# Kernel tuning notes

Measured on AMD Instinct MI355X. Metric: run time of the kernel, lower is better.

Reference implementation:

```python
import jax, jax.numpy as jnp
import numpy as np

N_HEAD = 8
TOKEN_CODIM = 4   # mixer token codimension; attention uses per-channel tokens (codim 1)
TEMP = 1.0
EPS = 1e-5


def instance_norm(x, w=None, b=None):
    # InstanceNorm2d: normalize each (sample, channel) over spatial dims
    mu = jnp.mean(x, axis=(-2, -1), keepdims=True)
    var = jnp.var(x, axis=(-2, -1), keepdims=True)
    y = (x - mu) * jax.lax.rsqrt(var + EPS)
    if w is not None:
        y = y * w[:, None, None] + b[:, None, None]
    return y


def spectral_conv(x, wr, wi, bias, out_hw):
    # x: (B, Cin, H, W); weight (Cin, Cout, m1, m2) complex; fft_norm='forward'
    B, Cin, H, W = x.shape
    Ho, Wo = out_hw
    w = wr + 1j * wi
    m1, m2 = wr.shape[2], wr.shape[3]
    h = m1 // 2
    xf = jnp.fft.rfft2(x, norm='forward')                  # (B, Cin, H, W//2+1)
    top = jnp.einsum('bixy,ioxy->boxy', xf[:, :, :h, :m2], w[:, :, :h])
    bot = jnp.einsum('bixy,ioxy->boxy', xf[:, :, H - h:, :m2], w[:, :, h:])
    of = jnp.zeros((B, wr.shape[1], Ho, Wo // 2 + 1), dtype=xf.dtype)
    of = of.at[:, :, :h, :m2].set(top)
    of = of.at[:, :, Ho - h:, :m2].set(bot)
    return jnp.fft.irfft2(of, s=(Ho, Wo), norm='forward') + bias[:, None, None]


def fft_resample(x, Ho, Wo):
    # Fourier-truncation resampling (used for the skip branch when the conv rescales)
    B, C, H, W = x.shape
    xf = jnp.fft.rfft2(x, norm='forward')
    h, wc = Ho // 2, Wo // 2 + 1
    of = jnp.zeros((B, C, Ho, wc), dtype=xf.dtype)
    of = of.at[:, :, :h].set(xf[:, :, :h, :wc])
    of = of.at[:, :, Ho - h:].set(xf[:, :, H - h:, :wc])
    return jnp.fft.irfft2(of, s=(Ho, Wo), norm='forward')


def fno_layer(x, wr, wi, bias, sw, sb, out_hw, norm=False, act=False):
    # one FNOBlocks layer: spectral conv (+optional instance norm) + 1x1 linear skip (+act)
    skip = jnp.einsum('bihw,oi->bohw', x, sw) + sb[:, None, None]
    if out_hw != tuple(x.shape[-2:]):
        skip = fft_resample(skip, *out_hw)
    xf = spectral_conv(x, wr, wi, bias, out_hw)
    if norm:
        xf = instance_norm(xf)
    y = xf + skip
    return jax.nn.gelu(y, approximate=False) if act else y


def to_heads(z, b):
    # '(b t) (a d) h w -> b a t (d h w)'
    bt, ad, h, w = z.shape
    t = bt // b
    z = z.reshape(b, t, N_HEAD, ad // N_HEAD, h, w)
    return jnp.transpose(z, (0, 2, 1, 3, 4, 5)).reshape(b, N_HEAD, t, -1)


def setup_inputs():
    key = jax.random.key(0)
    ks = jax.random.split(key, 12)
    b, C, H, W = 2, 128, 128, 128
    f = jax.random.normal
    return dict(
        x=f(ks[0], (b, C, H, W), jnp.float32),
        norm1_w=jnp.ones((1,)), norm1_b=jnp.zeros((1,)),
        kqv_wr=f(ks[1], (3, 1, N_HEAD, 16, 8)) * 0.02,
        kqv_wi=f(ks[2], (3, 1, N_HEAD, 16, 8)) * 0.02,
        kqv_bias=f(ks[3], (3, N_HEAD)) * 0.02,
        kqv_sw=f(ks[4], (3, N_HEAD, 1)) * 0.5,
        kqv_sb=jnp.zeros((3, N_HEAD)),
        p_wr=f(ks[5], (N_HEAD, 1, 32, 16)) * 0.02,
        p_wi=f(ks[6], (N_HEAD, 1, 32, 16)) * 0.02,
        p_bias=jnp.zeros((1,)),
        p_sw=f(ks[7], (1, N_HEAD)) * (1.0 / np.sqrt(N_HEAD)),
        p_sb=jnp.zeros((1,)),
        attn_norm_w=jnp.ones((1,)), attn_norm_b=jnp.zeros((1,)),
        norm2_w=jnp.ones((TOKEN_CODIM,)), norm2_b=jnp.zeros((TOKEN_CODIM,)),
        mix_wr=f(ks[8], (2, TOKEN_CODIM, TOKEN_CODIM, 32, 16)) * 0.02,
        mix_wi=f(ks[9], (2, TOKEN_CODIM, TOKEN_CODIM, 32, 16)) * 0.02,
        mix_bias=jnp.zeros((2, TOKEN_CODIM)),
        mix_sw=f(ks[10], (2, TOKEN_CODIM, TOKEN_CODIM)) * 0.5,
        mix_sb=jnp.zeros((2, TOKEN_CODIM)),
        mon_w=jnp.ones((TOKEN_CODIM,)), mon_b=jnp.zeros((TOKEN_CODIM,)),
    )


def reference(x, norm1_w, norm1_b, kqv_wr, kqv_wi, kqv_bias, kqv_sw, kqv_sb,
              p_wr, p_wi, p_bias, p_sw, p_sb, attn_norm_w, attn_norm_b,
              norm2_w, norm2_b, mix_wr, mix_wi, mix_bias, mix_sw, mix_sb,
              mon_w, mon_b):
    b, C, H, W = x.shape
    tokens = x.reshape(b * C, 1, H, W)                     # per-channel tokens
    tok_n = instance_norm(tokens, norm1_w, norm1_b)        # norm1

    # K, Q downsampled by scale=2; V at full resolution (kqv_modes = n_modes // 2)
    k = fno_layer(tok_n, kqv_wr[0], kqv_wi[0], kqv_bias[0], kqv_sw[0], kqv_sb[0], (H // 2, W // 2))
    q = fno_layer(tok_n, kqv_wr[1], kqv_wi[1], kqv_bias[1], kqv_sw[1], kqv_sb[1], (H // 2, W // 2))
    v = fno_layer(tok_n, kqv_wr[2], kqv_wi[2], kqv_bias[2], kqv_sw[2], kqv_sb[2], (H, W))

    kh, qh, vh = to_heads(k, b), to_heads(q, b), to_heads(v, b)
    scores = jnp.einsum('bati,basi->bats', qh, kh) / (np.float32(np.sqrt(kh.shape[-1])) * TEMP)
    probs = jax.nn.softmax(scores, axis=-1)                # (b, heads, t, t)
    attn = jnp.einsum('bats,basi->bati', probs, vh)        # (b, heads, C, H*W)
    attn = attn.reshape(b, N_HEAD, C, 1, H, W).transpose(0, 2, 1, 3, 4, 5).reshape(b * C, N_HEAD, H, W)

    attn = fno_layer(attn, p_wr, p_wi, p_bias, p_sw, p_sb, (H, W))   # proj heads -> codim 1
    attn = instance_norm(attn + tokens, attn_norm_w, attn_norm_b)

    # regroup channels into mixer tokens of codimension 4
    attn = attn.reshape(b * (C // TOKEN_CODIM), TOKEN_CODIM, H, W)
    h0 = instance_norm(attn, norm2_w, norm2_b)
    h1 = fno_layer(h0, mix_wr[0], mix_wi[0], mix_bias[0], mix_sw[0], mix_sb[0], (H, W), norm=True, act=True)
    h2 = fno_layer(h1, mix_wr[1], mix_wi[1], mix_bias[1], mix_sw[1], mix_sb[1], (H, W), norm=True)
    out = instance_norm(h2, mon_w, mon_b) + attn
    return out.reshape(b, C, H, W)
```

## Files before the change

kernel.cpp:

```cpp
#include <hip/hip_runtime.h>
#include <math.h>


#define NT 2112

__device__ __forceinline__ void blockReduce2(float& a, float& b, float* red){
  const int tid = threadIdx.x, n = blockDim.x;
  red[tid] = a; red[n+tid] = b;
  __syncthreads();
  for(int off=n>>1; off>0; off>>=1){
    if(tid<off){ red[tid]+=red[tid+off]; red[n+tid]+=red[n+tid+off]; }
    __syncthreads();
  }
  a = red[0]; b = red[n];
  __syncthreads();
}

__device__ __forceinline__ float2 cmul_add(float2 acc, float2 w, float2 x){
  acc.x += w.x*x.x - w.y*x.y;
  acc.y += w.x*x.y + w.y*x.x;
  return acc;
}

__global__ void k_tables(float2* __restrict__ CS){
  int a = blockIdx.x, b = threadIdx.x;
  int p = (a*b)&127;
  float t = (float)p * (1.0f/64.0f);
  CS[a*128+b] = make_float2(cospif(t), sinpif(t));
}

__global__ __launch_bounds__(256) void k_instats(
    const float* __restrict__ xin, const float* __restrict__ n1w,
    const float* __restrict__ n1b, float* __restrict__ a1, float* __restrict__ b1)
{
  __shared__ float red[512];
  const int m = blockIdx.x, t = threadIdx.x;
  const float* xp = xin + (size_t)m*16384;
  float s1=0.f, s2=0.f;
  for(int i=t;i<4096;i+=256){
    float4 v = ((const float4*)xp)[i];
    s1 += v.x+v.y+v.z+v.w;
    s2 += v.x*v.x+v.y*v.y+v.z*v.z+v.w*v.w;
  }
  blockReduce2(s1,s2,red);
  if(t==0){
    float mu = s1*(1.0f/16384.0f);
    float var = s2*(1.0f/16384.0f)-mu*mu;
    float a = n1w[0]*rsqrtf(var+1e-5f);
    a1[m] = a; b1[m] = n1b[0] - mu*a;
  }
}

__global__ __launch_bounds__(256) void k_p1(
    const float* __restrict__ xin, float* __restrict__ R1r, float* __restrict__ R1i,
    const float2* __restrict__ CS)
{
  __shared__ float xl[32*129];
  __shared__ float2 csl[4224];
  const int bid = blockIdx.x;
  const int m = bid>>2, yt = bid&3;
  const int t = threadIdx.x;
  for(int i=t;i<4224;i+=256) csl[i] = CS[i];
  {
    const float4* xp4 = (const float4*)(xin + (size_t)m*16384 + yt*4096);
    for(int i4=t;i4<1024;i4+=256){
      float4 v = xp4[i4];
      int y = i4>>5, n = (i4&31)*4;
      xl[y*129+n]=v.x; xl[y*129+n+1]=v.y; xl[y*129+n+2]=v.z; xl[y*129+n+3]=v.w;
    }
  }
  __syncthreads();
  const int yl = t&31, cg = t>>5;
  const int nc = (cg==0)?5:4;
  float ar[5]={0,0,0,0,0}, ai[5]={0,0,0,0,0};
  for(int n=0;n<128;n++){
    float xv = xl[yl*129+n];
    #pragma unroll
    for(int k=0;k<5;k++){
      if(k<nc){
        float2 cs = csl[(cg+8*k)*128+n];
        ar[k] += xv*cs.x;
        ai[k] -= xv*cs.y;
      }
    }
  }
  __syncthreads();
  #pragma unroll
  for(int k=0;k<5;k++){
    if(k<nc){
      int c = cg+8*k;
      xl[yl*33+c] = ar[k];
      xl[1056 + yl*33+c] = ai[k];
    }
  }
  __syncthreads();
  const int gb = m*4224 + yt*1056;
  for(int idx=t; idx<2112; idx+=256){
    if(idx<1056) R1r[gb+idx] = xl[idx];
    else         R1i[gb+idx-1056] = xl[idx];
  }
}

__global__ __launch_bounds__(704) void k_p2(
    const float* __restrict__ R1r, const float* __restrict__ R1i,
    const float2* __restrict__ CS, const float* __restrict__ a1,
    const float* __restrict__ n1b,
    float2* __restrict__ Xt2, float2* __restrict__ Xp)
{
  __shared__ float2 Rl[128*34];
  const int m = blockIdx.x, t = threadIdx.x;
  for(int idx=t; idx<4224; idx+=704){
    int y = idx/33, c = idx - y*33;
    Rl[y*34+c] = make_float2(R1r[m*4224+idx], R1i[m*4224+idx]);
  }
  __syncthreads();
  const float sc = a1[m]*(1.0f/16384.0f);
  const int r = t&63;
  const int ky = (r<32)? r : r+64;
  #pragma unroll
  for(int k=0;k<3;k++){
    int c = (t>>6) + 11*k;
    float ar=0.f, ai=0.f;
    for(int y=0;y<128;y++){
      float2 Rv = Rl[y*34+c];
      float2 cs = CS[128 + ((ky*y)&127)];
      ar += Rv.x*cs.x + Rv.y*cs.y;
      ai += Rv.y*cs.x - Rv.x*cs.y;
    }
    int j = r*33 + c;
    float vr = ar*sc, vi = ai*sc;
    if(j==0){ vr = n1b[0]; vi = 0.f; }
    Xt2[m*NT+j] = make_float2(vr, vi);
    if(c<16 && (r<16 || r>=48)){
      int rp = (r<16)? r : r-32;
      Xp[m*512 + rp*16 + c] = make_float2(vr, vi);
    }
  }
}

__global__ __launch_bounds__(256) void k_build_k(
  const float2* __restrict__ Xt2,
  const float* __restrict__ kqv_wr, const float* __restrict__ kqv_wi,
  const float* __restrict__ kqv_bias, const float* __restrict__ kqv_sw,
  const float* __restrict__ kqv_sb,
  float2* __restrict__ Kc)
{
  __shared__ float2 T[2112];
  __shared__ float2 Ks[2112];
  const int bid = blockIdx.x;
  const int m = bid & 255, o = bid >> 8;
  const int tid = threadIdx.x;
  for(int j=tid;j<2112;j+=256) T[j] = Xt2[m*NT+j];
  __syncthreads();
  const float swK = kqv_sw[o];
  const float swQ = kqv_sw[8+o];
  for(int j=tid;j<2112;j+=256){
    int r = j/33, c = j - r*33;
    float2 X = T[j];
    float2 K = make_float2(swK*X.x, swK*X.y);
    if(c<8){
      int wrow = (r<8)? r : ((r>=56)? r-48 : -1);
      if(wrow>=0)
        K = cmul_add(K, make_float2(kqv_wr[(o*16+wrow)*8+c], kqv_wi[(o*16+wrow)*8+c]), X);
    }
    if(j==0) K.x += kqv_bias[o] + kqv_sb[o];
    Ks[j] = K;
  }
  __syncthreads();
  const size_t ob = ((size_t)(m*8+o))*NT;
  for(int j=tid;j<2112;j+=256){
    int r = j/33, c = j - r*33;
    float2 K = Ks[j];
    float wsc = 128.0f;
    if(c==0 || c==32){
      int pj = ((64-r)&63)*33 + c;
      float2 K2 = Ks[pj];
      K = make_float2(0.5f*(K.x+K2.x), 0.5f*(K.y-K2.y));
      wsc = 64.0f;
    }
    float ar = swQ, ai = 0.f;
    if(c<8){
      int wrow = (r<8)? r : ((r>=56)? r-48 : -1);
      if(wrow>=0){ ar += kqv_wr[((8+o)*16+wrow)*8+c]; ai += kqv_wi[((8+o)*16+wrow)*8+c]; }
    }
    float2 out = make_float2(wsc*(ar*K.x + ai*K.y), wsc*(ar*K.y - ai*K.x));
    if(j==0) out = make_float2(0.f, 0.f);
    Kc[ob+j] = out;
  }
}

__global__ __launch_bounds__(256) void k_scores(
  const float2* __restrict__ Xt2, const float2* __restrict__ Kc,
  float* __restrict__ Pp)
{
  __shared__ float Qs[64*52];
  __shared__ float Ks[64*52];
  const int bid = blockIdx.x;
  const int fq = bid&15, st = (bid>>4)&1, tt = (bid>>5)&1, h = (bid>>6)&7, b = bid>>9;
  const int t = threadIdx.x;
  const int tg = t>>4, sg = t&15;
  const int t0 = tt*64, s0 = st*64;
  const int f2base = fq*132;
  float acc[4][4];
  #pragma unroll
  for(int i=0;i<4;i++)
    #pragma unroll
    for(int j=0;j<4;j++) acc[i][j]=0.f;
  for(int sub=0; sub<6; sub++){
    __syncthreads();
    const int fo = f2base + sub*22;
    for(int idx=t; idx<1408; idx+=256){
      int rl = idx/22, f2 = idx - rl*22;
      float2 q = Xt2[(size_t)(b*128 + t0+rl)*NT + fo + f2];
      ((float2*)(Qs + rl*52))[f2] = q;
      float2 kk = Kc[((size_t)((b*128 + s0+rl)*8+h))*NT + fo + f2];
      ((float2*)(Ks + rl*52))[f2] = kk;
    }
    __syncthreads();
    #pragma unroll
    for(int f4=0; f4<11; f4++){
      float4 qv[4], kv[4];
      #pragma unroll
      for(int i=0;i<4;i++) qv[i] = *(const float4*)&Qs[(tg+16*i)*52 + f4*4];
      #pragma unroll
      for(int j=0;j<4;j++) kv[j] = *(const float4*)&Ks[(sg+16*j)*52 + f4*4];
      #pragma unroll
      for(int i=0;i<4;i++)
        #pragma unroll
        for(int j=0;j<4;j++)
          acc[i][j] += qv[i].x*kv[j].x + qv[i].y*kv[j].y
                     + qv[i].z*kv[j].z + qv[i].w*kv[j].w;
    }
  }
  #pragma unroll
  for(int i=0;i<4;i++){
    int tg2 = t0 + tg + 16*i;
    #pragma unroll
    for(int j=0;j<4;j++){
      int s = s0 + sg + 16*j;
      Pp[(size_t)fq*262144 + ((size_t)((b*8+h)*128+tg2))*128 + s] = acc[i][j];
    }
  }
}

__global__ __launch_bounds__(64) void k_softmax(const float* __restrict__ Pp,
                                                float* __restrict__ P){
  const int row = blockIdx.x, tid = threadIdx.x;
  size_t o = (size_t)row*128;
  float v0=0.f, v1=0.f;
  #pragma unroll
  for(int q=0;q<16;q++){
    v0 += Pp[(size_t)q*262144 + o + tid];
    v1 += Pp[(size_t)q*262144 + o + tid + 64];
  }
  float mx = fmaxf(v0,v1);
  for(int off=32; off; off>>=1) mx = fmaxf(mx, __shfl_xor(mx, off));
  float e0 = expf(v0-mx), e1 = expf(v1-mx);
  float s = e0+e1;
  for(int off=32; off; off>>=1) s += __shfl_xor(s, off);
  float inv = 1.0f/s;
  P[o+tid] = e0*inv; P[o+tid+64] = e1*inv;
}

__global__ __launch_bounds__(256) void k_peff(const float* __restrict__ P,
   const float* __restrict__ p_sw, const float* __restrict__ kqv_sw,
   const float* __restrict__ a1, float* __restrict__ PAT)
{
  const int i = blockIdx.x*256 + threadIdx.x;
  const int b = i>>14, rem = i&16383;
  const int tch = rem>>7, s = rem&127;
  float acc=0.f;
  for(int hh=0; hh<8; hh++){
    float a = p_sw[hh]*kqv_sw[16+hh];
    acc += a * P[(((size_t)(b*8+hh))<<14) + rem];
  }
  PAT[((size_t)(b*128+s))*128 + tch] = acc * a1[b*128+s];
}

__global__ __launch_bounds__(128) void k_pbeta(const float* __restrict__ P,
   const float* __restrict__ p_sw, const float* __restrict__ kqv_sw,
   const float* __restrict__ b1, float* __restrict__ pbeta)
{
  __shared__ float red[128];
  const int bid = blockIdx.x;
  const int b = bid>>7, tch = bid&127;
  const int s = threadIdx.x;
  float acc=0.f;
  for(int hh=0; hh<8; hh++){
    float a = p_sw[hh]*kqv_sw[16+hh];
    acc += a * P[((size_t)((b*8+hh)*128+tch))*128 + s];
  }
  acc *= b1[b*128+s];
  red[s] = acc; __syncthreads();
  for(int off=64; off>0; off>>=1){
    if(s<off) red[s]+=red[s+off];
    __syncthreads();
  }
  if(s==0) pbeta[bid] = red[0];
}

__global__ __launch_bounds__(256) void k_zp(const float* __restrict__ P,
  const float* __restrict__ Xp, float* __restrict__ Zc)
{
  __shared__ float Pt[32*17];
  __shared__ float Xs[32*256];
  const int bid = blockIdx.x;
  const int b = bid>>8;
  const int r8 = bid&255;
  const int jt = r8>>6, o = (r8>>3)&7, ct = r8&7;
  const int t = threadIdx.x;
  const int tc = t>>6, tj = t&63;
  const int c0 = ct*16;
  float4 acc[4];
  #pragma unroll
  for(int k=0;k<4;k++) acc[k] = make_float4(0.f,0.f,0.f,0.f);
  for(int scn=0; scn<4; scn++){
    __syncthreads();
    for(int idx=t; idx<512; idx+=256){
      int sl = idx&31, cl = idx>>5;
      Pt[sl*17+cl] = P[((size_t)((b*8+o)*128 + c0+cl))*128 + scn*32+sl];
    }
    for(int q=t; q<2048; q+=256){
      int sl = q>>6, p4 = q&63;
      ((float4*)Xs)[q] = ((const float4*)Xp)[((size_t)(b*128 + scn*32+sl))*256 + jt*64 + p4];
    }
    __syncthreads();
    for(int sl=0; sl<32; sl++){
      float4 xv = ((const float4*)Xs)[sl*64+tj];
      #pragma unroll
      for(int k=0;k<4;k++){
        float pa = Pt[sl*17 + tc*4+k];
        acc[k].x += pa*xv.x; acc[k].y += pa*xv.y;
        acc[k].z += pa*xv.z; acc[k].w += pa*xv.w;
      }
    }
  }
  #pragma unroll
  for(int k=0;k<4;k++){
    ((float4*)Zc)[((size_t)((b*8+o)*128 + c0+tc*4+k))*256 + jt*64 + tj] = acc[k];
  }
}

__global__ __launch_bounds__(256) void k_corr(
  const float* __restrict__ Zc,
  const float* __restrict__ kqv_wr, const float* __restrict__ kqv_wi,
  const float* __restrict__ kqv_bias, const float* __restrict__ kqv_sw, const float* __restrict__ kqv_sb,
  const float* __restrict__ p_wr, const float* __restrict__ p_wi,
  const float* __restrict__ p_bias, const float* __restrict__ p_sw, const float* __restrict__ p_sb,
  float2* __restrict__ Bc)
{
  const float2* Z2 = (const float2*)Zc;
  const int m = blockIdx.x;
  const int b = m>>7, cix = m&127;
  const int tid = threadIdx.x;
  for(int j=tid; j<512; j+=256){
    int r = j>>4, c = j&15;
    int ky = (r<16)? r : 96+r;
    float accr=0.f, acci=0.f;
    int rp = -1;
    if(c==0){ int kyp = (128-ky)&127; rp = (kyp<16)? kyp : ((kyp>=112)? kyp-96 : -1); }
    for(int o=0;o<8;o++){
      size_t zoff = ((size_t)((b*8+o)*128 + cix))*512;
      float2 z = Z2[zoff+j];
      float cvr=0.f, cvi=0.f;
      bool inV = (c<8) && (ky<8 || ky>=120);
      if(inV){
        int vrow = (ky<8)? ky : 8+(ky-120);
        float wr = kqv_wr[((16+o)*16+vrow)*8+c], wi = kqv_wi[((16+o)*16+vrow)*8+c];
        cvr = wr*z.x - wi*z.y; cvi = wr*z.y + wi*z.x;
      }
      float ar = cvr, ai = cvi;
      if(c==0){
        float pvr=0.f, pvi=0.f;
        int kyp = (128-ky)&127;
        bool pInV = (kyp<8 || kyp>=120);
        if(pInV && rp>=0){
          int vrow = (kyp<8)? kyp : 8+(kyp-120);
          float2 z2 = Z2[zoff + rp*16];
          float wr = kqv_wr[((16+o)*16+vrow)*8], wi = kqv_wi[((16+o)*16+vrow)*8];
          pvr = wr*z2.x - wi*z2.y; pvi = wr*z2.y + wi*z2.x;
        }
        ar = 0.5f*(cvr + pvr);
        ai = 0.5f*(cvi - pvi);
      }
      float sv = kqv_sw[16+o];
      float Dv = kqv_bias[16+o] + kqv_sb[16+o];
      float atr = sv*z.x + ar + ((j==0)? Dv : 0.f);
      float ati = sv*z.y + ai;
      float psw = p_sw[o];
      accr += psw*ar;  acci += psw*ai;
      float wpr = p_wr[(o*32+r)*16+c], wpi = p_wi[(o*32+r)*16+c];
      accr += wpr*atr - wpi*ati;
      acci += wpr*ati + wpi*atr;
      if(j==0) accr += psw*Dv;
    }
    if(j==0) accr += p_bias[0] + p_sb[0];
    Bc[m*512+j] = make_float2(accr, acci);
  }
}

__global__ __launch_bounds__(256) void k_attn_gemm(
  const float* __restrict__ PAT, const float* __restrict__ xin,
  const float* __restrict__ pbeta, float* __restrict__ y0g)
{
  __shared__ float PAs[32*33];
  __shared__ float Xs[32*256];
  const int bid = blockIdx.x;
  const int b = bid>>8, ct = (bid>>6)&3, pt = bid&63;
  const int t = threadIdx.x;
  const int tc = t>>6, tp = t&63;
  float4 acc[8];
  #pragma unroll
  for(int k=0;k<8;k++) acc[k] = make_float4(0.f,0.f,0.f,0.f);
  for(int sc4=0; sc4<4; sc4++){
    __syncthreads();
    for(int idx=t; idx<1024; idx+=256){
      int sl = idx>>5, cl = idx&31;
      PAs[sl*33+cl] = PAT[((size_t)(b*128 + sc4*32+sl))*128 + ct*32+cl];
    }
    for(int q=t; q<2048; q+=256){
      int sl = q>>6, p4 = q&63;
      ((float4*)Xs)[q] =
        ((const float4*)xin)[((size_t)(b*128 + sc4*32+sl))*4096 + pt*64 + p4];
    }
    __syncthreads();
    for(int sl=0; sl<32; sl++){
      float4 xv = ((const float4*)Xs)[sl*64+tp];
      #pragma unroll
      for(int k=0;k<8;k++){
        float pa = PAs[sl*33 + tc*8+k];
        acc[k].x += pa*xv.x; acc[k].y += pa*xv.y;
        acc[k].z += pa*xv.z; acc[k].w += pa*xv.w;
      }
    }
  }
  #pragma unroll
  for(int k=0;k<8;k++){
    int c = ct*32 + tc*8 + k;
    float pb = pbeta[b*128+c];
    float4 o = acc[k];
    o.x += pb; o.y += pb; o.z += pb; o.w += pb;
    ((float4*)y0g)[((size_t)(b*128+c))*4096 + pt*64 + tp] = o;
  }
}

__global__ __launch_bounds__(512) void k_epi0(
  const float* __restrict__ y0g, const float* __restrict__ xin,
  const float2* __restrict__ Bc,
  const float2* __restrict__ CS,
  const float* __restrict__ awp, const float* __restrict__ abp,
  const float* __restrict__ n2w, const float* __restrict__ n2b,
  float* __restrict__ attn, float* __restrict__ a2, float* __restrict__ b2,
  float2* __restrict__ Hc)
{
  __shared__ float2 Bcl[512];
  __shared__ float2 V[128*17];
  __shared__ float V2p[128*132];
  __shared__ float red[1024];
  const int m = blockIdx.x, t = threadIdx.x;
  Bcl[t] = Bc[m*512+t];
  __syncthreads();
  #pragma unroll
  for(int k=0;k<4;k++){
    int idx = t + 512*k;
    int mm = idx>>4, c = idx&15;
    float vr=0.f, vi=0.f;
    for(int r=0;r<32;r++){
      int ky = (r<16)? r : 96+r;
      float2 bc = Bcl[r*16+c];
      float2 cs = CS[128 + ((ky*mm)&127)];
      vr += bc.x*cs.x - bc.y*cs.y;
      vi += bc.x*cs.y + bc.y*cs.x;
    }
    float w = (c==0)?1.0f:2.0f;
    V[mm*17+c] = make_float2(vr*w, vi*w);
  }
  __syncthreads();
  {
    const int n = t&127, mm0 = t>>7;
    float2 csr[16];
    #pragma unroll
    for(int c=0;c<16;c++) csr[c] = CS[c*128+n];
    for(int k=0;k<32;k++){
      int mm = mm0 + 4*k;
      float cv = 0.f;
      #pragma unroll
      for(int c=0;c<16;c++){
        float2 v2 = V[mm*17+c];
        cv += v2.x*csr[c].x - v2.y*csr[c].y;
      }
      V2p[mm*132+n] = cv;
    }
  }
  __syncthreads();
  const float4* x4 = (const float4*)(xin + (size_t)m*16384);
  const float4* g4 = (const float4*)(y0g + (size_t)m*16384);
  float4* V24 = (float4*)V2p;
  float s1=0.f, s2=0.f;
  for(int k=0;k<8;k++){
    int q = t + 512*k;
    int row = q>>5, c4 = q&31;
    float4 xv = x4[q], gv = g4[q], cc = V24[row*33+c4];
    float4 v;
    v.x = xv.x+gv.x+cc.x; v.y = xv.y+gv.y+cc.y;
    v.z = xv.z+gv.z+cc.z; v.w = xv.w+gv.w+cc.w;
    s1 += v.x+v.y+v.z+v.w;
    s2 += v.x*v.x+v.y*v.y+v.z*v.z+v.w*v.w;
    V24[row*33+c4] = v;
  }
  blockReduce2(s1,s2,red);
  float mu = s1*(1.0f/16384.0f);
  float var = s2*(1.0f/16384.0f)-mu*mu;
  float rs = rsqrtf(var+1e-5f);
  float aw = awp[0], ab = abp[0];
  float4* at4 = (float4*)(attn + (size_t)m*16384);
  for(int k=0;k<8;k++){
    int q = t + 512*k;
    int row = q>>5, c4 = q&31;
    float4 v = V24[row*33+c4];
    float4 ov;
    ov.x = (v.x-mu)*rs*aw + ab;
    ov.y = (v.y-mu)*rs*aw + ab;
    ov.z = (v.z-mu)*rs*aw + ab;
    ov.w = (v.w-mu)*rs*aw + ab;
    at4[q] = ov;
  }
  float va = aw*aw*var/(var+1e-5f);
  float al = n2w[m&3]*rsqrtf(va+1e-5f);
  if(t==0){ a2[m] = al; b2[m] = n2b[m&3] - ab*al; }
  __syncthreads();
  {
    const int yl = t&31, c = t>>5;
    for(int yc=0; yc<4; yc++){
      int y = yc*32+yl;
      float ar=0.f, ai=0.f;
      for(int n=0;n<128;n++){
        float zv = V2p[y*132+n];
        float2 cs = CS[c*128+n];
        ar += zv*cs.x; ai -= zv*cs.y;
      }
      V[y*17+c] = make_float2(ar, ai);
    }
  }
  __syncthreads();
  {
    const float scl = al*rs*aw*(1.0f/16384.0f);
    int idx = t;
    int r = idx>>4, c = idx&15;
    int ky = (r<16)? r : 96+r;
    float hr=0.f, hi=0.f;
    for(int y=0;y<128;y++){
      float2 Rv = V[y*17+c];
      float2 cs = CS[128 + ((ky*y)&127)];
      hr += Rv.x*cs.x + Rv.y*cs.y;
      hi += Rv.y*cs.x - Rv.x*cs.y;
    }
    float2 o = make_float2(hr*scl, hi*scl);
    if(idx==0) o = make_float2(n2b[m&3], 0.f);
    Hc[m*512+idx] = o;
  }
}

__global__ __launch_bounds__(256) void k_mixc(
  const float2* __restrict__ Hc,
  const float* __restrict__ wr0, const float* __restrict__ wi0,
  float2* __restrict__ Sn)
{
  __shared__ float2 Sl[512];
  __shared__ float red[512];
  const int mb = blockIdx.x;
  const int g = mb&63, o = mb>>6;
  const int t = threadIdx.x;
  for(int j=t;j<512;j+=256){
    int r = j>>4, c = j&15;
    float ar=0.f, ai=0.f;
    for(int i2=0;i2<4;i2++){
      float2 h = Hc[(g*4+i2)*512 + j];
      float wr = wr0[((i2*4+o)*32+r)*16+c], wi = wi0[((i2*4+o)*32+r)*16+c];
      ar += wr*h.x - wi*h.y; ai += wr*h.y + wi*h.x;
    }
    Sl[j] = make_float2(ar, ai);
  }
  __syncthreads();
  float vs=0.f, dummy=0.f;
  for(int j=t;j<512;j+=256){
    int c=j&15;
    if(c>=1) vs += 2.0f*(Sl[j].x*Sl[j].x + Sl[j].y*Sl[j].y);
  }
  if(t<32){
    int ky = (t<16)? (t+1) : (96+t);
    float ar=0.f, ai=0.f;
    if(ky<16){ ar=Sl[ky*16].x; ai=Sl[ky*16].y; }
    else if(ky>=112){ int r=ky-96; ar=Sl[r*16].x; ai=Sl[r*16].y; }
    int kyp = 128-ky;
    float br2=0.f, bi2=0.f;
    if(kyp<16){ br2=Sl[kyp*16].x; bi2=Sl[kyp*16].y; }
    else if(kyp>=112){ int r=kyp-96; br2=Sl[r*16].x; bi2=Sl[r*16].y; }
    float pr = 0.5f*(ar+br2), pi = 0.5f*(ai-bi2);
    vs += pr*pr + pi*pi;
  }
  blockReduce2(vs, dummy, red);
  float rs2 = rsqrtf(vs + 1e-5f);
  for(int j=t;j<512;j+=256){
    float2 s = Sl[j];
    if(j==0) Sn[(g*4+o)*512+j] = make_float2(0.f,0.f);
    else     Sn[(g*4+o)*512+j] = make_float2(s.x*rs2, s.y*rs2);
  }
}

__global__ __launch_bounds__(512) void k_mixinv(
  const float2* __restrict__ Sn, const float* __restrict__ inmaps,
  const float* __restrict__ a2, const float* __restrict__ b2,
  const float* __restrict__ msw, const float* __restrict__ msb,
  const float2* __restrict__ CS, const int dogelu,
  float2* __restrict__ HcOut,
  const float* __restrict__ addsrc, const float* __restrict__ mw,
  const float* __restrict__ mbv,
  float* __restrict__ outp)
{
  __shared__ float2 Sl[512];
  __shared__ float2 V[128*17];
  __shared__ float V2p[128*132];
  __shared__ float red[1024];
  const int mb = blockIdx.x;
  const int g = mb&63, o = mb>>6;
  const int mmap = g*4+o;
  const int t = threadIdx.x;
  float cw[4]; float cb = msb[o];
  #pragma unroll
  for(int i=0;i<4;i++){
    float al = a2 ? a2[g*4+i] : 1.0f;
    float be = b2 ? b2[g*4+i] : 0.0f;
    float sw = msw[o*4+i];
    cw[i] = sw*al; cb += sw*be;
  }
  Sl[t] = Sn[mmap*512+t];
  __syncthreads();
  #pragma unroll
  for(int k=0;k<4;k++){
    int idx = t + 512*k;
    int mm = idx>>4, c = idx&15;
    float vr=0.f, vi=0.f;
    for(int r=0;r<32;r++){
      int ky = (r<16)? r : 96+r;
      float2 bc = Sl[r*16+c];
      float2 cs = CS[128 + ((ky*mm)&127)];
      vr += bc.x*cs.x - bc.y*cs.y;
      vi += bc.x*cs.y + bc.y*cs.x;
    }
    float w = (c==0)?1.0f:2.0f;
    V[mm*17+c] = make_float2(vr*w, vi*w);
  }
  __syncthreads();
  {
    const int n = t&127, mm0 = t>>7;
    float2 csr[16];
    #pragma unroll
    for(int c=0;c<16;c++) csr[c] = CS[c*128+n];
    for(int k=0;k<32;k++){
      int mm = mm0 + 4*k;
      float cv = 0.f;
      #pragma unroll
      for(int c=0;c<16;c++){
        float2 v2 = V[mm*17+c];
        cv += v2.x*csr[c].x - v2.y*csr[c].y;
      }
      V2p[mm*132+n] = cv;
    }
  }
  __syncthreads();
  const float4* in4 = (const float4*)(inmaps + (size_t)(g*4)*16384);
  float4* V24 = (float4*)V2p;
  float4* o4 = (float4*)(outp + (size_t)mmap*16384);
  float s1=0.f, s2=0.f;
  for(int k=0;k<8;k++){
    int q = t + 512*k;
    int row = q>>5, c4 = q&31;
    float4 v0 = in4[q], v1 = in4[4096+q], v2 = in4[8192+q], v3 = in4[12288+q];
    float4 cc = V24[row*33+c4];
    float4 ov;
    ov.x = cb + cw[0]*v0.x + cw[1]*v1.x + cw[2]*v2.x + cw[3]*v3.x + cc.x;
    ov.y = cb + cw[0]*v0.y + cw[1]*v1.y + cw[2]*v2.y + cw[3]*v3.y + cc.y;
    ov.z = cb + cw[0]*v0.z + cw[1]*v1.z + cw[2]*v2.z + cw[3]*v3.z + cc.z;
    ov.w = cb + cw[0]*v0.w + cw[1]*v1.w + cw[2]*v2.w + cw[3]*v3.w + cc.w;
    if(dogelu){
      ov.x = 0.5f*ov.x*(1.0f+erff(ov.x*0.70710678118f));
      ov.y = 0.5f*ov.y*(1.0f+erff(ov.y*0.70710678118f));
      ov.z = 0.5f*ov.z*(1.0f+erff(ov.z*0.70710678118f));
      ov.w = 0.5f*ov.w*(1.0f+erff(ov.w*0.70710678118f));
    }
    if(addsrc){
      s1 += ov.x+ov.y+ov.z+ov.w;
      s2 += ov.x*ov.x+ov.y*ov.y+ov.z*ov.z+ov.w*ov.w;
      V24[row*33+c4] = ov;
    } else {
      o4[q] = ov;
      if(HcOut) V24[row*33+c4] = ov;
    }
  }
  if(addsrc){
    blockReduce2(s1,s2,red);
    float mu = s1*(1.0f/16384.0f);
    float var = s2*(1.0f/16384.0f)-mu*mu;
    float rs = rsqrtf(var+1e-5f);
    float w = mw[o], b = mbv[o];
    const float4* a4 = (const float4*)(addsrc + (size_t)mmap*16384);
    for(int k=0;k<8;k++){
      int q = t + 512*k;
      int row = q>>5, c4 = q&31;
      float4 v = V24[row*33+c4], av = a4[q];
      float4 ov;
      ov.x = (v.x-mu)*rs*w + b + av.x;
      ov.y = (v.y-mu)*rs*w + b + av.y;
      ov.z = (v.z-mu)*rs*w + b + av.z;
      ov.w = (v.w-mu)*rs*w + b + av.w;
      o4[q] = ov;
    }
  }
  if(HcOut){
    __syncthreads();
    {
      const int yl = t&31, c = t>>5;
      for(int yc=0; yc<4; yc++){
        int y = yc*32+yl;
        float ar=0.f, ai=0.f;
        for(int n=0;n<128;n++){
          float zv = V2p[y*132+n];
          float2 cs = CS[c*128+n];
          ar += zv*cs.x; ai -= zv*cs.y;
        }
        V[y*17+c] = make_float2(ar, ai);
      }
    }
    __syncthreads();
    {
      int idx = t;
      int r = idx>>4, c = idx&15;
      int ky = (r<16)? r : 96+r;
      float hr=0.f, hi=0.f;
      for(int y=0;y<128;y++){
        float2 Rv = V[y*17+c];
        float2 cs = CS[128 + ((ky*y)&127)];
        hr += Rv.x*cs.x + Rv.y*cs.y;
        hi += Rv.y*cs.x - Rv.x*cs.y;
      }
      HcOut[mmap*512+idx] = make_float2(hr*(1.0f/16384.0f), hi*(1.0f/16384.0f));
    }
  }
}

extern "C" void kernel_launch(void* const* d_in, const int* in_sizes, int n_in,
                              void* d_out, int out_size, void* d_ws, size_t ws_size,
                              hipStream_t stream)
{
  const float* x        = (const float*)d_in[0];
  const float* norm1_w  = (const float*)d_in[1];
  const float* norm1_b  = (const float*)d_in[2];
  const float* kqv_wr   = (const float*)d_in[3];
  const float* kqv_wi   = (const float*)d_in[4];
  const float* kqv_bias = (const float*)d_in[5];
  const float* kqv_sw   = (const float*)d_in[6];
  const float* kqv_sb   = (const float*)d_in[7];
  const float* p_wr     = (const float*)d_in[8];
  const float* p_wi     = (const float*)d_in[9];
  const float* p_bias   = (const float*)d_in[10];
  const float* p_sw     = (const float*)d_in[11];
  const float* p_sb     = (const float*)d_in[12];
  const float* attn_norm_w = (const float*)d_in[13];
  const float* attn_norm_b = (const float*)d_in[14];
  const float* norm2_w  = (const float*)d_in[15];
  const float* norm2_b  = (const float*)d_in[16];
  const float* mix_wr   = (const float*)d_in[17];
  const float* mix_wi   = (const float*)d_in[18];
  const float* mix_sw   = (const float*)d_in[20];
  const float* mix_sb   = (const float*)d_in[21];
  const float* mon_w    = (const float*)d_in[22];
  const float* mon_b    = (const float*)d_in[23];
  float* out = (float*)d_out;

  const size_t NEED = (size_t)26576128 * sizeof(float);
  if(ws_size < NEED) return;

  float* ws = (float*)d_ws;
  size_t off = 0;
  float2* CS  = (float2*)(ws + off); off += 32768;
  float* a1   = ws + off; off += 256;
  float* b1   = ws + off; off += 256;
  float* a2   = ws + off; off += 256;
  float* b2   = ws + off; off += 256;
  float* pbeta= ws + off; off += 256;
  float2* Xt2 = (float2*)(ws + off); off += 1081344;
  float* pool = ws + off; off += 17301504;
  float* P    = ws + off; off += 262144;
  float* PAT  = ws + off; off += 32768;
  float2* Xp  = (float2*)(ws + off); off += 262144;
  float* Zc   = ws + off; off += 2097152;
  float2* Bc  = (float2*)(ws + off); off += 262144;
  float* attn = ws + off; off += 4194304;
  float2* Hc  = (float2*)(ws + off); off += 524288;
  float2* Sn  = (float2*)(ws + off); off += 524288;

  float* Pp   = attn;

  float2* Kc = (float2*)pool;
  float* R1r = pool + 8650752;
  float* R1i = pool + 8650752 + 1081344;
  float* y0g = pool;
  float* h1  = pool + 4325376;

  k_tables<<<dim3(128), dim3(128), 0, stream>>>(CS);
  k_instats<<<dim3(256), dim3(256), 0, stream>>>(x, norm1_w, norm1_b, a1, b1);
  k_p1<<<dim3(1024), dim3(256), 0, stream>>>(x, R1r, R1i, CS);
  k_p2<<<dim3(256), dim3(704), 0, stream>>>(R1r, R1i, CS, a1, norm1_b, Xt2, Xp);
  k_build_k<<<dim3(2048), dim3(256), 0, stream>>>(Xt2, kqv_wr, kqv_wi, kqv_bias,
                                                  kqv_sw, kqv_sb, Kc);
  k_scores<<<dim3(1024), dim3(256), 0, stream>>>(Xt2, Kc, Pp);
  k_softmax<<<dim3(2048), dim3(64), 0, stream>>>(Pp, P);
  k_peff<<<dim3(128), dim3(256), 0, stream>>>(P, p_sw, kqv_sw, a1, PAT);
  k_pbeta<<<dim3(256), dim3(128), 0, stream>>>(P, p_sw, kqv_sw, b1, pbeta);
  k_zp<<<dim3(512), dim3(256), 0, stream>>>(P, (const float*)Xp, Zc);
  k_corr<<<dim3(256), dim3(256), 0, stream>>>(Zc, kqv_wr, kqv_wi, kqv_bias, kqv_sw, kqv_sb,
                                              p_wr, p_wi, p_bias, p_sw, p_sb, Bc);
  k_attn_gemm<<<dim3(512), dim3(256), 0, stream>>>(PAT, x, pbeta, y0g);
  k_epi0<<<dim3(256), dim3(512), 0, stream>>>(y0g, x, Bc, CS, attn_norm_w, attn_norm_b,
                                              norm2_w, norm2_b, attn, a2, b2, Hc);
  k_mixc<<<dim3(256), dim3(256), 0, stream>>>(Hc, mix_wr, mix_wi, Sn);
  k_mixinv<<<dim3(256), dim3(512), 0, stream>>>(Sn, attn, a2, b2, mix_sw, mix_sb, CS, 1,
                                                Hc, (const float*)nullptr,
                                                (const float*)nullptr, (const float*)nullptr, h1);
  k_mixc<<<dim3(256), dim3(256), 0, stream>>>(Hc, mix_wr+8192, mix_wi+8192, Sn);
  k_mixinv<<<dim3(256), dim3(512), 0, stream>>>(Sn, h1, (const float*)nullptr, (const float*)nullptr,
                                                mix_sw+16, mix_sb+4, CS, 0,
                                                (float2*)nullptr, attn, mon_w, mon_b, out);
}
```

Measured before the change: 390.4 us.

## Fuse spectral forward transforms with K build, and Z product with correction

Three kernels (row DFT, column DFT, per-head K construction) become one per-channel kernel, k_spec. The R1 and Xt2 intermediates now stay in shared memory instead of going through global memory, and the kernel loops over the 8 heads internally. Separately, the P·Xp product is fused with the correction kernel: Z is accumulated in registers and staged in LDS instead of writing and re-reading the large Zc buffer. This removes global round-trips and launches. The cost is far fewer, much larger blocks (256 blocks with about 134KB of LDS each), which lowers parallelism in the heavy Kc-writing stage.

```diff
diff --git a/kernel.cpp b/kernel.cpp
--- a/kernel.cpp
+++ b/kernel.cpp
@@ -51,141 +51,122 @@
   }
 }
 
-__global__ __launch_bounds__(256) void k_p1(
-    const float* __restrict__ xin, float* __restrict__ R1r, float* __restrict__ R1i,
-    const float2* __restrict__ CS)
-{
-  __shared__ float xl[32*129];
-  __shared__ float2 csl[4224];
-  const int bid = blockIdx.x;
-  const int m = bid>>2, yt = bid&3;
-  const int t = threadIdx.x;
-  for(int i=t;i<4224;i+=256) csl[i] = CS[i];
+__global__ __launch_bounds__(512) void k_spec(
+    const float* __restrict__ xin, const float2* __restrict__ CS,
+    const float* __restrict__ a1, const float* __restrict__ n1b,
+    const float* __restrict__ kqv_wr, const float* __restrict__ kqv_wi,
+    const float* __restrict__ kqv_bias, const float* __restrict__ kqv_sw,
+    const float* __restrict__ kqv_sb,
+    float2* __restrict__ Xt2, float2* __restrict__ Xp, float2* __restrict__ Kc)
+{
+  __shared__ float xl[128*129];
+  __shared__ float2 Rst[128*33];
+  __shared__ float2 Xt2l[2112];
+  __shared__ float2 Ksl[2112];
+  const int m = blockIdx.x, t = threadIdx.x;
   {
-    const float4* xp4 = (const float4*)(xin + (size_t)m*16384 + yt*4096);
-    for(int i4=t;i4<1024;i4+=256){
+    const float4* xp4 = (const float4*)(xin + (size_t)m*16384);
+    for(int i4=t;i4<4096;i4+=512){
       float4 v = xp4[i4];
       int y = i4>>5, n = (i4&31)*4;
       xl[y*129+n]=v.x; xl[y*129+n+1]=v.y; xl[y*129+n+2]=v.z; xl[y*129+n+3]=v.w;
     }
   }
   __syncthreads();
-  const int yl = t&31, cg = t>>5;
-  const int nc = (cg==0)?5:4;
-  float ar[5]={0,0,0,0,0}, ai[5]={0,0,0,0,0};
-  for(int n=0;n<128;n++){
-    float xv = xl[yl*129+n];
+  {
+    const int yl = t&31, cgrp = t>>5;
+    const int nc = (cgrp==0)?3:2;
+    for(int yt=0; yt<4; yt++){
+      int y = yt*32 + yl;
+      float ar[3]={0,0,0}, ai[3]={0,0,0};
+      for(int n=0;n<128;n++){
+        float xv = xl[y*129+n];
+        #pragma unroll
+        for(int k=0;k<3;k++){
+          if(k<nc){
+            float2 cs = CS[(cgrp+16*k)*128+n];
+            ar[k] += xv*cs.x;
+            ai[k] -= xv*cs.y;
+          }
+        }
+      }
+      #pragma unroll
+      for(int k=0;k<3;k++){
+        if(k<nc){
+          int c = cgrp+16*k;
+          Rst[y*33+c] = make_float2(ar[k], ai[k]);
+        }
+      }
+    }
+  }
+  __syncthreads();
+  {
+    const float sc = a1[m]*(1.0f/16384.0f);
+    const int r = t&63, cg = t>>6;
+    const int ky = (r<32)? r : r+64;
+    const int nk = (cg==0)?5:4;
     #pragma unroll
     for(int k=0;k<5;k++){
-      if(k<nc){
-        float2 cs = csl[(cg+8*k)*128+n];
-        ar[k] += xv*cs.x;
-        ai[k] -= xv*cs.y;
-      }
-    }
-  }
-  __syncthreads();
-  #pragma unroll
-  for(int k=0;k<5;k++){
-    if(k<nc){
-      int c = cg+8*k;
-      xl[yl*33+c] = ar[k];
-      xl[1056 + yl*33+c] = ai[k];
-    }
-  }
-  __syncthreads();
-  const int gb = m*4224 + yt*1056;
-  for(int idx=t; idx<2112; idx+=256){
-    if(idx<1056) R1r[gb+idx] = xl[idx];
-    else         R1i[gb+idx-1056] = xl[idx];
-  }
-}
-
-__global__ __launch_bounds__(704) void k_p2(
-    const float* __restrict__ R1r, const float* __restrict__ R1i,
-    const float2* __restrict__ CS, const float* __restrict__ a1,
-    const float* __restrict__ n1b,
-    float2* __restrict__ Xt2, float2* __restrict__ Xp)
-{
-  __shared__ float2 Rl[128*34];
-  const int m = blockIdx.x, t = threadIdx.x;
-  for(int idx=t; idx<4224; idx+=704){
-    int y = idx/33, c = idx - y*33;
-    Rl[y*34+c] = make_float2(R1r[m*4224+idx], R1i[m*4224+idx]);
-  }
-  __syncthreads();
-  const float sc = a1[m]*(1.0f/16384.0f);
-  const int r = t&63;
-  const int ky = (r<32)? r : r+64;
-  #pragma unroll
-  for(int k=0;k<3;k++){
-    int c = (t>>6) + 11*k;
-    float ar=0.f, ai=0.f;
-    for(int y=0;y<128;y++){
-      float2 Rv = Rl[y*34+c];
-      float2 cs = CS[128 + ((ky*y)&127)];
-      ar += Rv.x*cs.x + Rv.y*cs.y;
-      ai += Rv.y*cs.x - Rv.x*cs.y;
-    }
-    int j = r*33 + c;
-    float vr = ar*sc, vi = ai*sc;
-    if(j==0){ vr = n1b[0]; vi = 0.f; }
-    Xt2[m*NT+j] = make_float2(vr, vi);
-    if(c<16 && (r<16 || r>=48)){
-      int rp = (r<16)? r : r-32;
-      Xp[m*512 + rp*16 + c] = make_float2(vr, vi);
-    }
-  }
-}
-
-__global__ __launch_bounds__(256) void k_build_k(
-  const float2* __restrict__ Xt2,
-  const float* __restrict__ kqv_wr, const float* __restrict__ kqv_wi,
-  const float* __restrict__ kqv_bias, const float* __restrict__ kqv_sw,
-  const float* __restrict__ kqv_sb,
-  float2* __restrict__ Kc)
-{
-  __shared__ float2 T[2112];
-  __shared__ float2 Ks[2112];
-  const int bid = blockIdx.x;
-  const int m = bid & 255, o = bid >> 8;
-  const int tid = threadIdx.x;
-  for(int j=tid;j<2112;j+=256) T[j] = Xt2[m*NT+j];
-  __syncthreads();
-  const float swK = kqv_sw[o];
-  const float swQ = kqv_sw[8+o];
-  for(int j=tid;j<2112;j+=256){
-    int r = j/33, c = j - r*33;
-    float2 X = T[j];
-    float2 K = make_float2(swK*X.x, swK*X.y);
-    if(c<8){
-      int wrow = (r<8)? r : ((r>=56)? r-48 : -1);
-      if(wrow>=0)
-        K = cmul_add(K, make_float2(kqv_wr[(o*16+wrow)*8+c], kqv_wi[(o*16+wrow)*8+c]), X);
-    }
-    if(j==0) K.x += kqv_bias[o] + kqv_sb[o];
-    Ks[j] = K;
-  }
-  __syncthreads();
-  const size_t ob = ((size_t)(m*8+o))*NT;
-  for(int j=tid;j<2112;j+=256){
-    int r = j/33, c = j - r*33;
-    float2 K = Ks[j];
-    float wsc = 128.0f;
-    if(c==0 || c==32){
-      int pj = ((64-r)&63)*33 + c;
-      float2 K2 = Ks[pj];
-      K = make_float2(0.5f*(K.x+K2.x), 0.5f*(K.y-K2.y));
-      wsc = 64.0f;
-    }
-    float ar = swQ, ai = 0.f;
-    if(c<8){
-      int wrow = (r<8)? r : ((r>=56)? r-48 : -1);
-      if(wrow>=0){ ar += kqv_wr[((8+o)*16+wrow)*8+c]; ai += kqv_wi[((8+o)*16+wrow)*8+c]; }
-    }
-    float2 out = make_float2(wsc*(ar*K.x + ai*K.y), wsc*(ar*K.y - ai*K.x));
-    if(j==0) out = make_float2(0.f, 0.f);
-    Kc[ob+j] = out;
+      if(k<nk){
+        int c = cg + 8*k;
+        float ar=0.f, ai=0.f;
+        for(int y=0;y<128;y++){
+          float2 Rv = Rst[y*33+c];
+          float2 cs = CS[128 + ((ky*y)&127)];
+          ar += Rv.x*cs.x + Rv.y*cs.y;
+          ai += Rv.y*cs.x - Rv.x*cs.y;
+        }
+        int j = r*33 + c;
+        float vr = ar*sc, vi = ai*sc;
+        if(j==0){ vr = n1b[0]; vi = 0.f; }
+        float2 val = make_float2(vr, vi);
+        Xt2[m*NT+j] = val;
+        Xt2l[j] = val;
+        if(c<16 && (r<16 || r>=48)){
+          int rp = (r<16)? r : r-32;
+          Xp[m*512 + rp*16 + c] = val;
+        }
+      }
+    }
+  }
+  __syncthreads();
+  for(int o=0;o<8;o++){
+    const float swK = kqv_sw[o];
+    const float swQ = kqv_sw[8+o];
+    for(int j=t;j<2112;j+=512){
+      int r = j/33, c = j - r*33;
+      float2 X = Xt2l[j];
+      float2 K = make_float2(swK*X.x, swK*X.y);
+      if(c<8){
+        int wrow = (r<8)? r : ((r>=56)? r-48 : -1);
+        if(wrow>=0)
+          K = cmul_add(K, make_float2(kqv_wr[(o*16+wrow)*8+c], kqv_wi[(o*16+wrow)*8+c]), X);
+      }
+      if(j==0) K.x += kqv_bias[o] + kqv_sb[o];
+      Ksl[j] = K;
+    }
+    __syncthreads();
+    const size_t ob = ((size_t)(m*8+o))*NT;
+    for(int j=t;j<2112;j+=512){
+      int r = j/33, c = j - r*33;
+      float2 K = Ksl[j];
+      float wsc = 128.0f;
+      if(c==0 || c==32){
+        int pj = ((64-r)&63)*33 + c;
+        float2 K2 = Ksl[pj];
+        K = make_float2(0.5f*(K.x+K2.x), 0.5f*(K.y-K2.y));
+        wsc = 64.0f;
+      }
+      float ar = swQ, ai = 0.f;
+      if(c<8){
+        int wrow = (r<8)? r : ((r>=56)? r-48 : -1);
+        if(wrow>=0){ ar += kqv_wr[((8+o)*16+wrow)*8+c]; ai += kqv_wi[((8+o)*16+wrow)*8+c]; }
+      }
+      float2 out = make_float2(wsc*(ar*K.x + ai*K.y), wsc*(ar*K.y - ai*K.x));
+      if(j==0) out = make_float2(0.f, 0.f);
+      Kc[ob+j] = out;
+    }
+    __syncthreads();
   }
 }
 
@@ -299,75 +280,64 @@
   if(s==0) pbeta[bid] = red[0];
 }
 
-__global__ __launch_bounds__(256) void k_zp(const float* __restrict__ P,
-  const float* __restrict__ Xp, float* __restrict__ Zc)
-{
-  __shared__ float Pt[32*17];
-  __shared__ float Xs[32*256];
-  const int bid = blockIdx.x;
-  const int b = bid>>8;
-  const int r8 = bid&255;
-  const int jt = r8>>6, o = (r8>>3)&7, ct = r8&7;
-  const int t = threadIdx.x;
-  const int tc = t>>6, tj = t&63;
-  const int c0 = ct*16;
-  float4 acc[4];
-  #pragma unroll
-  for(int k=0;k<4;k++) acc[k] = make_float4(0.f,0.f,0.f,0.f);
-  for(int scn=0; scn<4; scn++){
-    __syncthreads();
-    for(int idx=t; idx<512; idx+=256){
-      int sl = idx&31, cl = idx>>5;
-      Pt[sl*17+cl] = P[((size_t)((b*8+o)*128 + c0+cl))*128 + scn*32+sl];
-    }
-    for(int q=t; q<2048; q+=256){
-      int sl = q>>6, p4 = q&63;
-      ((float4*)Xs)[q] = ((const float4*)Xp)[((size_t)(b*128 + scn*32+sl))*256 + jt*64 + p4];
-    }
-    __syncthreads();
-    for(int sl=0; sl<32; sl++){
-      float4 xv = ((const float4*)Xs)[sl*64+tj];
-      #pragma unroll
-      for(int k=0;k<4;k++){
-        float pa = Pt[sl*17 + tc*4+k];
-        acc[k].x += pa*xv.x; acc[k].y += pa*xv.y;
-        acc[k].z += pa*xv.z; acc[k].w += pa*xv.w;
-      }
-    }
-  }
-  #pragma unroll
-  for(int k=0;k<4;k++){
-    ((float4*)Zc)[((size_t)((b*8+o)*128 + c0+tc*4+k))*256 + jt*64 + tj] = acc[k];
-  }
-}
-
-__global__ __launch_bounds__(256) void k_corr(
-  const float* __restrict__ Zc,
+__global__ __launch_bounds__(512) void k_zcorr(
+  const float* __restrict__ P, const float2* __restrict__ Xp,
   const float* __restrict__ kqv_wr, const float* __restrict__ kqv_wi,
   const float* __restrict__ kqv_bias, const float* __restrict__ kqv_sw, const float* __restrict__ kqv_sb,
   const float* __restrict__ p_wr, const float* __restrict__ p_wi,
   const float* __restrict__ p_bias, const float* __restrict__ p_sw, const float* __restrict__ p_sb,
   float2* __restrict__ Bc)
 {
-  const float2* Z2 = (const float2*)Zc;
+  __shared__ float4 Xs4[4096];
+  __shared__ float Pl[1024];
   const int m = blockIdx.x;
   const int b = m>>7, cix = m&127;
-  const int tid = threadIdx.x;
-  for(int j=tid; j<512; j+=256){
+  const int t = threadIdx.x;
+  const int j = t;
+  for(int idx=t; idx<1024; idx+=512){
+    int o = idx>>7, s = idx&127;
+    Pl[idx] = P[((size_t)((b*8+o)*128 + cix))*128 + s];
+  }
+  float2 z[8];
+  #pragma unroll
+  for(int o=0;o<8;o++) z[o] = make_float2(0.f,0.f);
+  const float2* Xs = (const float2*)Xs4;
+  for(int st=0; st<8; st++){
+    __syncthreads();
+    for(int q=t; q<4096; q+=512){
+      int sl = q>>8, f4 = q&255;
+      Xs4[q] = ((const float4*)(Xp + (size_t)(b*128 + st*16 + sl)*512))[f4];
+    }
+    __syncthreads();
+    for(int sl=0; sl<16; sl++){
+      int s = st*16 + sl;
+      float2 xv = Xs[sl*512 + j];
+      #pragma unroll
+      for(int o=0;o<8;o++){
+        float p = Pl[o*128+s];
+        z[o].x += p*xv.x; z[o].y += p*xv.y;
+      }
+    }
+  }
+  __syncthreads();
+  float2* Zl = (float2*)Xs4;
+  #pragma unroll
+  for(int o=0;o<8;o++) Zl[o*512 + j] = z[o];
+  __syncthreads();
+  {
     int r = j>>4, c = j&15;
     int ky = (r<16)? r : 96+r;
     float accr=0.f, acci=0.f;
     int rp = -1;
     if(c==0){ int kyp = (128-ky)&127; rp = (kyp<16)? kyp : ((kyp>=112)? kyp-96 : -1); }
     for(int o=0;o<8;o++){
-      size_t zoff = ((size_t)((b*8+o)*128 + cix))*512;
-      float2 z = Z2[zoff+j];
+      float2 zv = Zl[o*512 + j];
       float cvr=0.f, cvi=0.f;
       bool inV = (c<8) && (ky<8 || ky>=120);
       if(inV){
         int vrow = (ky<8)? ky : 8+(ky-120);
         float wr = kqv_wr[((16+o)*16+vrow)*8+c], wi = kqv_wi[((16+o)*16+vrow)*8+c];
-        cvr = wr*z.x - wi*z.y; cvi = wr*z.y + wi*z.x;
+        cvr = wr*zv.x - wi*zv.y; cvi = wr*zv.y + wi*zv.x;
       }
       float ar = cvr, ai = cvi;
       if(c==0){
@@ -376,7 +346,7 @@
         bool pInV = (kyp<8 || kyp>=120);
         if(pInV && rp>=0){
           int vrow = (kyp<8)? kyp : 8+(kyp-120);
-          float2 z2 = Z2[zoff + rp*16];
+          float2 z2 = Zl[o*512 + rp*16];
           float wr = kqv_wr[((16+o)*16+vrow)*8], wi = kqv_wi[((16+o)*16+vrow)*8];
           pvr = wr*z2.x - wi*z2.y; pvi = wr*z2.y + wi*z2.x;
         }
@@ -385,8 +355,8 @@
       }
       float sv = kqv_sw[16+o];
       float Dv = kqv_bias[16+o] + kqv_sb[16+o];
-      float atr = sv*z.x + ar + ((j==0)? Dv : 0.f);
-      float ati = sv*z.y + ai;
+      float atr = sv*zv.x + ar + ((j==0)? Dv : 0.f);
+      float ati = sv*zv.y + ai;
       float psw = p_sw[o];
       accr += psw*ar;  acci += psw*ai;
       float wpr = p_wr[(o*32+r)*16+c], wpi = p_wi[(o*32+r)*16+c];
@@ -794,33 +764,30 @@
   float* P    = ws + off; off += 262144;
   float* PAT  = ws + off; off += 32768;
   float2* Xp  = (float2*)(ws + off); off += 262144;
-  float* Zc   = ws + off; off += 2097152;
+  float* Zc_unused = ws + off; off += 2097152;
   float2* Bc  = (float2*)(ws + off); off += 262144;
   float* attn = ws + off; off += 4194304;
   float2* Hc  = (float2*)(ws + off); off += 524288;
   float2* Sn  = (float2*)(ws + off); off += 524288;
+  (void)Zc_unused;
 
   float* Pp   = attn;
 
   float2* Kc = (float2*)pool;
-  float* R1r = pool + 8650752;
-  float* R1i = pool + 8650752 + 1081344;
   float* y0g = pool;
   float* h1  = pool + 4325376;
 
   k_tables<<<dim3(128), dim3(128), 0, stream>>>(CS);
   k_instats<<<dim3(256), dim3(256), 0, stream>>>(x, norm1_w, norm1_b, a1, b1);
-  k_p1<<<dim3(1024), dim3(256), 0, stream>>>(x, R1r, R1i, CS);
-  k_p2<<<dim3(256), dim3(704), 0, stream>>>(R1r, R1i, CS, a1, norm1_b, Xt2, Xp);
-  k_build_k<<<dim3(2048), dim3(256), 0, stream>>>(Xt2, kqv_wr, kqv_wi, kqv_bias,
-                                                  kqv_sw, kqv_sb, Kc);
+  k_spec<<<dim3(256), dim3(512), 0, stream>>>(x, CS, a1, norm1_b,
+                                              kqv_wr, kqv_wi, kqv_bias, kqv_sw, kqv_sb,
+                                              Xt2, Xp, Kc);
   k_scores<<<dim3(1024), dim3(256), 0, stream>>>(Xt2, Kc, Pp);
   k_softmax<<<dim3(2048), dim3(64), 0, stream>>>(Pp, P);
   k_peff<<<dim3(128), dim3(256), 0, stream>>>(P, p_sw, kqv_sw, a1, PAT);
   k_pbeta<<<dim3(256), dim3(128), 0, stream>>>(P, p_sw, kqv_sw, b1, pbeta);
-  k_zp<<<dim3(512), dim3(256), 0, stream>>>(P, (const float*)Xp, Zc);
-  k_corr<<<dim3(256), dim3(256), 0, stream>>>(Zc, kqv_wr, kqv_wi, kqv_bias, kqv_sw, kqv_sb,
-                                              p_wr, p_wi, p_bias, p_sw, p_sb, Bc);
+  k_zcorr<<<dim3(256), dim3(512), 0, stream>>>(P, Xp, kqv_wr, kqv_wi, kqv_bias, kqv_sw, kqv_sb,
+                                               p_wr, p_wi, p_bias, p_sw, p_sb, Bc);
   k_attn_gemm<<<dim3(512), dim3(256), 0, stream>>>(PAT, x, pbeta, y0g);
   k_epi0<<<dim3(256), dim3(512), 0, stream>>>(y0g, x, Bc, CS, attn_norm_w, attn_norm_b,
                                               norm2_w, norm2_b, attn, a2, b2, Hc);
```

New measurement: 444.6 us. +13.9%, slower.

## Fuse probability-weighted spectral mix into correction kernel, dropping Zc buffer

Applied to the files above, without the earlier changes.

Merges k_zp (P times Xp contraction into Zc) and k_corr into one kernel, k_zcorr. Each block now computes all 8 heads for one (b, channel) in registers, stages the result in shared memory and applies the correction directly. This removes the global write and read of the 8 MB Zc intermediate and one launch. In exchange the grid shrinks to 256 blocks of 512 threads using 64 KB of shared memory, which cuts parallelism and occupancy, and each block re-reads all of Xp for its batch.

```diff
diff --git a/kernel.cpp b/kernel.cpp
--- a/kernel.cpp
+++ b/kernel.cpp
@@ -299,75 +299,64 @@
   if(s==0) pbeta[bid] = red[0];
 }
 
-__global__ __launch_bounds__(256) void k_zp(const float* __restrict__ P,
-  const float* __restrict__ Xp, float* __restrict__ Zc)
-{
-  __shared__ float Pt[32*17];
-  __shared__ float Xs[32*256];
-  const int bid = blockIdx.x;
-  const int b = bid>>8;
-  const int r8 = bid&255;
-  const int jt = r8>>6, o = (r8>>3)&7, ct = r8&7;
-  const int t = threadIdx.x;
-  const int tc = t>>6, tj = t&63;
-  const int c0 = ct*16;
-  float4 acc[4];
-  #pragma unroll
-  for(int k=0;k<4;k++) acc[k] = make_float4(0.f,0.f,0.f,0.f);
-  for(int scn=0; scn<4; scn++){
-    __syncthreads();
-    for(int idx=t; idx<512; idx+=256){
-      int sl = idx&31, cl = idx>>5;
-      Pt[sl*17+cl] = P[((size_t)((b*8+o)*128 + c0+cl))*128 + scn*32+sl];
-    }
-    for(int q=t; q<2048; q+=256){
-      int sl = q>>6, p4 = q&63;
-      ((float4*)Xs)[q] = ((const float4*)Xp)[((size_t)(b*128 + scn*32+sl))*256 + jt*64 + p4];
-    }
-    __syncthreads();
-    for(int sl=0; sl<32; sl++){
-      float4 xv = ((const float4*)Xs)[sl*64+tj];
-      #pragma unroll
-      for(int k=0;k<4;k++){
-        float pa = Pt[sl*17 + tc*4+k];
-        acc[k].x += pa*xv.x; acc[k].y += pa*xv.y;
-        acc[k].z += pa*xv.z; acc[k].w += pa*xv.w;
-      }
-    }
-  }
-  #pragma unroll
-  for(int k=0;k<4;k++){
-    ((float4*)Zc)[((size_t)((b*8+o)*128 + c0+tc*4+k))*256 + jt*64 + tj] = acc[k];
-  }
-}
-
-__global__ __launch_bounds__(256) void k_corr(
-  const float* __restrict__ Zc,
+__global__ __launch_bounds__(512) void k_zcorr(
+  const float* __restrict__ P, const float2* __restrict__ Xp,
   const float* __restrict__ kqv_wr, const float* __restrict__ kqv_wi,
   const float* __restrict__ kqv_bias, const float* __restrict__ kqv_sw, const float* __restrict__ kqv_sb,
   const float* __restrict__ p_wr, const float* __restrict__ p_wi,
   const float* __restrict__ p_bias, const float* __restrict__ p_sw, const float* __restrict__ p_sb,
   float2* __restrict__ Bc)
 {
-  const float2* Z2 = (const float2*)Zc;
+  __shared__ float4 Xs4[4096];
+  __shared__ float Pl[1024];
   const int m = blockIdx.x;
   const int b = m>>7, cix = m&127;
-  const int tid = threadIdx.x;
-  for(int j=tid; j<512; j+=256){
+  const int t = threadIdx.x;
+  const int j = t;
+  for(int idx=t; idx<1024; idx+=512){
+    int o = idx>>7, s = idx&127;
+    Pl[idx] = P[((size_t)((b*8+o)*128 + cix))*128 + s];
+  }
+  float2 z[8];
+  #pragma unroll
+  for(int o=0;o<8;o++) z[o] = make_float2(0.f,0.f);
+  const float2* Xs = (const float2*)Xs4;
+  for(int st=0; st<8; st++){
+    __syncthreads();
+    for(int q=t; q<4096; q+=512){
+      int sl = q>>8, f4 = q&255;
+      Xs4[q] = ((const float4*)(Xp + (size_t)(b*128 + st*16 + sl)*512))[f4];
+    }
+    __syncthreads();
+    for(int sl=0; sl<16; sl++){
+      int s = st*16 + sl;
+      float2 xv = Xs[sl*512 + j];
+      #pragma unroll
+      for(int o=0;o<8;o++){
+        float p = Pl[o*128+s];
+        z[o].x += p*xv.x; z[o].y += p*xv.y;
+      }
+    }
+  }
+  __syncthreads();
+  float2* Zl = (float2*)Xs4;
+  #pragma unroll
+  for(int o=0;o<8;o++) Zl[o*512 + j] = z[o];
+  __syncthreads();
+  {
     int r = j>>4, c = j&15;
     int ky = (r<16)? r : 96+r;
     float accr=0.f, acci=0.f;
     int rp = -1;
     if(c==0){ int kyp = (128-ky)&127; rp = (kyp<16)? kyp : ((kyp>=112)? kyp-96 : -1); }
     for(int o=0;o<8;o++){
-      size_t zoff = ((size_t)((b*8+o)*128 + cix))*512;
-      float2 z = Z2[zoff+j];
+      float2 zv = Zl[o*512 + j];
       float cvr=0.f, cvi=0.f;
       bool inV = (c<8) && (ky<8 || ky>=120);
       if(inV){
         int vrow = (ky<8)? ky : 8+(ky-120);
         float wr = kqv_wr[((16+o)*16+vrow)*8+c], wi = kqv_wi[((16+o)*16+vrow)*8+c];
-        cvr = wr*z.x - wi*z.y; cvi = wr*z.y + wi*z.x;
+        cvr = wr*zv.x - wi*zv.y; cvi = wr*zv.y + wi*zv.x;
       }
       float ar = cvr, ai = cvi;
       if(c==0){
@@ -376,7 +365,7 @@
         bool pInV = (kyp<8 || kyp>=120);
         if(pInV && rp>=0){
           int vrow = (kyp<8)? kyp : 8+(kyp-120);
-          float2 z2 = Z2[zoff + rp*16];
+          float2 z2 = Zl[o*512 + rp*16];
           float wr = kqv_wr[((16+o)*16+vrow)*8], wi = kqv_wi[((16+o)*16+vrow)*8];
           pvr = wr*z2.x - wi*z2.y; pvi = wr*z2.y + wi*z2.x;
         }
@@ -385,8 +374,8 @@
       }
       float sv = kqv_sw[16+o];
       float Dv = kqv_bias[16+o] + kqv_sb[16+o];
-      float atr = sv*z.x + ar + ((j==0)? Dv : 0.f);
-      float ati = sv*z.y + ai;
+      float atr = sv*zv.x + ar + ((j==0)? Dv : 0.f);
+      float ati = sv*zv.y + ai;
       float psw = p_sw[o];
       accr += psw*ar;  acci += psw*ai;
       float wpr = p_wr[(o*32+r)*16+c], wpi = p_wi[(o*32+r)*16+c];
@@ -794,11 +783,12 @@
   float* P    = ws + off; off += 262144;
   float* PAT  = ws + off; off += 32768;
   float2* Xp  = (float2*)(ws + off); off += 262144;
-  float* Zc   = ws + off; off += 2097152;
+  float* Zc_unused = ws + off; off += 2097152;
   float2* Bc  = (float2*)(ws + off); off += 262144;
   float* attn = ws + off; off += 4194304;
   float2* Hc  = (float2*)(ws + off); off += 524288;
   float2* Sn  = (float2*)(ws + off); off += 524288;
+  (void)Zc_unused;
 
   float* Pp   = attn;
 
@@ -818,9 +808,8 @@
   k_softmax<<<dim3(2048), dim3(64), 0, stream>>>(Pp, P);
   k_peff<<<dim3(128), dim3(256), 0, stream>>>(P, p_sw, kqv_sw, a1, PAT);
   k_pbeta<<<dim3(256), dim3(128), 0, stream>>>(P, p_sw, kqv_sw, b1, pbeta);
-  k_zp<<<dim3(512), dim3(256), 0, stream>>>(P, (const float*)Xp, Zc);
-  k_corr<<<dim3(256), dim3(256), 0, stream>>>(Zc, kqv_wr, kqv_wi, kqv_bias, kqv_sw, kqv_sb,
-                                              p_wr, p_wi, p_bias, p_sw, p_sb, Bc);
+  k_zcorr<<<dim3(256), dim3(512), 0, stream>>>(P, Xp, kqv_wr, kqv_wi, kqv_bias, kqv_sw, kqv_sb,
+                                               p_wr, p_wi, p_bias, p_sw, p_sb, Bc);
   k_attn_gemm<<<dim3(512), dim3(256), 0, stream>>>(PAT, x, pbeta, y0g);
   k_epi0<<<dim3(256), dim3(512), 0, stream>>>(y0g, x, Bc, CS, attn_norm_w, attn_norm_b,
                                               norm2_w, norm2_b, attn, a2, b2, Hc);
```

New measurement: 386.3 us. About the same (-1.0%).
